# Optimization experiments

Hardware: AMD Instinct MI355X
Metric: run time of the kernel (lower is better)

The kernel has to match this reference:

```python
import jax, jax.numpy as jnp
import numpy as np
import math

DIM = 2048; H = 16; QR = 1536; KVR = 512; DN = 128; DR = 64; DV = 128
BS = 4; S = 1024
QK_HEAD = DN + DR  # 192


def _rms(x, w, eps=1e-6):
    v = jnp.mean(x * x, axis=-1, keepdims=True)
    return w * (x * jax.lax.rsqrt(v + eps))


def _rope_cos_sin(seq_len, dim):
    inv_freq = 1.0 / (10000.0 ** (jnp.arange(0, dim, 2, dtype=jnp.float32) / dim))
    t = jnp.arange(seq_len, dtype=jnp.float32)
    freqs = jnp.einsum('s,d->sd', t, inv_freq)
    freqs = jnp.concatenate([freqs, freqs], axis=-1)  # [S, dim]
    return jnp.cos(freqs), jnp.sin(freqs)


def _rotate_half(x):
    x1, x2 = jnp.split(x, 2, axis=-1)
    return jnp.concatenate([-x2, x1], axis=-1)


def setup_inputs() -> dict:
    key = jax.random.key(0)
    ks = jax.random.split(key, 12)
    sd = 0.02
    x = jax.random.normal(ks[0], (BS, S, DIM), dtype=jnp.float32)
    # causal additive mask [b, s, t]
    i = jnp.arange(S)
    causal = jnp.where(i[:, None] >= i[None, :], 0.0, -1e9).astype(jnp.float32)
    mask = jnp.broadcast_to(causal, (BS, S, S))
    return {
        'x': x,
        'mask': mask,
        'wq_a_w': jax.random.normal(ks[1], (QR, DIM)) * sd,
        'wq_a_b': jnp.zeros((QR,), jnp.float32),
        'q_norm_w': jnp.ones((QR,), jnp.float32),
        'wq_b_w': jax.random.normal(ks[2], (H * QK_HEAD, QR)) * sd,
        'wq_b_b': jnp.zeros((H * QK_HEAD,), jnp.float32),
        'wkv_a_w': jax.random.normal(ks[3], (KVR + DR, DIM)) * sd,
        'wkv_a_b': jnp.zeros((KVR + DR,), jnp.float32),
        'kv_norm_w': jnp.ones((KVR,), jnp.float32),
        'wkv_b_w': jax.random.normal(ks[4], (H * (DN + DV), KVR)) * sd,
        'wo_w': jax.random.normal(ks[5], (DIM, H * DV)) * sd,
        'wo_b': jnp.zeros((DIM,), jnp.float32),
    }


def reference(x, mask, wq_a_w, wq_a_b, q_norm_w, wq_b_w, wq_b_b,
              wkv_a_w, wkv_a_b, kv_norm_w, wkv_b_w, wo_w, wo_b):
    bs, seq_len, _ = x.shape
    # Q low-rank path
    q = x @ wq_a_w.T + wq_a_b                     # [b,s,QR]
    q = _rms(q, q_norm_w)
    q = q @ wq_b_w.T + wq_b_b                     # [b,s,H*192]
    q = q.reshape(bs, seq_len, H, QK_HEAD)
    q_nope, q_pe = q[..., :DN], q[..., DN:]       # [b,s,h,128], [b,s,h,64]
    # compressed KV path
    kv = x @ wkv_a_w.T + wkv_a_b                  # [b,s,KVR+64]
    c, k_pe = kv[..., :KVR], kv[..., KVR:]        # [b,s,512], [b,s,64]
    # RoPE on the rope sub-dims
    cos, sin = _rope_cos_sin(seq_len, DR)         # [s,64]
    cos4 = cos[None, :, None, :]
    sin4 = sin[None, :, None, :]
    q_pe = q_pe * cos4 + _rotate_half(q_pe) * sin4
    k_pe4 = k_pe[:, :, None, :]
    k_pe = (k_pe4 * cos4 + _rotate_half(k_pe4) * sin4)[:, :, 0, :]  # [b,s,64]
    # weight absorption: wkv_b viewed [H, DN+DV, KVR]
    wkv_b = wkv_b_w.reshape(H, DN + DV, KVR)
    q_abs = jnp.einsum('bshd,hdc->bshc', q_nope, wkv_b[:, :DN])      # [b,s,h,512]
    c_n = _rms(c, kv_norm_w)                                         # [b,t,512]
    scores = (jnp.einsum('bshc,btc->bsht', q_abs, c_n)
              + jnp.einsum('bshr,btr->bsht', q_pe, k_pe)) / math.sqrt(QK_HEAD)
    scores = scores + mask[:, :, None, :]
    scores = jax.nn.softmax(scores, axis=-1)
    o = jnp.einsum('bsht,btc->bshc', scores, c_n)                    # [b,s,h,512]
    o = jnp.einsum('bshc,hdc->bshd', o, wkv_b[:, -DV:])              # [b,s,h,128]
    o = o.reshape(bs, seq_len, H * DV)
    return o @ wo_w.T + wo_b
```

## Files before the change

### kernel.cpp

```cpp
#include <hip/hip_runtime.h>


typedef __attribute__((ext_vector_type(8))) short bf16x8;
typedef __attribute__((ext_vector_type(4))) float f32x4;
typedef __attribute__((ext_vector_type(4))) int i32x4;
typedef unsigned short ushort_t;
typedef unsigned int uint32;

typedef const __attribute__((address_space(1))) void* gas_ptr;
typedef __attribute__((address_space(3))) void* las_ptr;

#define DEV __device__ __forceinline__
#define WAITVM(N) asm volatile("s_waitcnt vmcnt(" #N ")" ::: "memory")

DEV float b2f(ushort_t u) { return __uint_as_float(((uint32)u) << 16); }
DEV ushort_t f2b(float f) {
  uint32 u = __float_as_uint(f);
  return (ushort_t)((u + 0x7fffu + ((u >> 16) & 1u)) >> 16);
}
DEV uint32 pkb(float lo, float hi) { return (uint32)f2b(lo) | ((uint32)f2b(hi) << 16); }

DEV void c4seg(const float4* __restrict__ in, ushort4* __restrict__ out, int i, int n4) {
  if (i < n4) {
    float4 v = in[i];
    ushort4 o; o.x = f2b(v.x); o.y = f2b(v.y); o.z = f2b(v.z); o.w = f2b(v.w);
    out[i] = o;
  }
}
DEV void vbseg(const float* __restrict__ in, ushort_t* __restrict__ out, int i4, int dofs) {
  int c4 = i4 & 127, d = (i4 >> 7) & 127, h = i4 >> 14;
  const float4 v = *(const float4*)(in + ((long)(h * 256 + dofs + d)) * 512 + c4 * 4);
  ushort4 o; o.x = f2b(v.x); o.y = f2b(v.y); o.z = f2b(v.z); o.w = f2b(v.w);
  ((ushort4*)out)[i4] = o;
}
__global__ __launch_bounds__(256) void castall_k(
    const float* __restrict__ x, const float* __restrict__ wq_a_w,
    const float* __restrict__ wkv_a_w, const float* __restrict__ wq_b_w,
    const float* __restrict__ wo_w, const float* __restrict__ wkv_b_w,
    ushort_t* __restrict__ xb, ushort_t* __restrict__ wcomb,
    ushort_t* __restrict__ wqb, ushort_t* __restrict__ wo,
    ushort_t* __restrict__ wkvbv, ushort_t* __restrict__ wkvbn) {
  int blk = blockIdx.x, tid = threadIdx.x;
  if (blk < 8192) {
    c4seg((const float4*)x, (ushort4*)xb, blk * 256 + tid, 2097152);
  } else if (blk < 11264) {
    c4seg((const float4*)wq_a_w, (ushort4*)wcomb, (blk - 8192) * 256 + tid, 786432);
  } else if (blk < 12416) {
    c4seg((const float4*)wkv_a_w, (ushort4*)(wcomb + 1536 * 2048),
          (blk - 11264) * 256 + tid, 294912);
  } else if (blk < 17024) {
    c4seg((const float4*)wq_b_w, (ushort4*)wqb, (blk - 12416) * 256 + tid, 1179648);
  } else if (blk < 21120) {
    c4seg((const float4*)wo_w, (ushort4*)wo, (blk - 17024) * 256 + tid, 1048576);
  } else if (blk < 22144) {
    vbseg(wkv_b_w, wkvbv, (blk - 21120) * 256 + tid, 128);
  } else {
    vbseg(wkv_b_w, wkvbn, (blk - 22144) * 256 + tid, 0);
  }
}

DEV float block_reduce_sum(float v, float* sbuf) {
#pragma unroll
  for (int d = 32; d >= 1; d >>= 1) v += __shfl_xor(v, d);
  if ((threadIdx.x & 63) == 0) sbuf[threadIdx.x >> 6] = v;
  __syncthreads();
  return sbuf[0] + sbuf[1] + sbuf[2] + sbuf[3];
}

__global__ __launch_bounds__(256) void rms_1536_k(const float* __restrict__ in,
                                                  ushort_t* __restrict__ out,
                                                  const float* __restrict__ w) {
  __shared__ float sbuf[4];
  long row = blockIdx.x;
  const float* p = in + row * 1536;
  float v[6]; float ss = 0.f;
#pragma unroll
  for (int i = 0; i < 6; ++i) { v[i] = p[threadIdx.x + i * 256]; ss += v[i] * v[i]; }
  ss = block_reduce_sum(ss, sbuf);
  float sc = rsqrtf(ss * (1.0f / 1536.0f) + 1e-6f);
#pragma unroll
  for (int i = 0; i < 6; ++i) {
    int c = threadIdx.x + i * 256;
    out[row * 1536 + c] = f2b(v[i] * sc * w[c]);
  }
}

__global__ __launch_bounds__(512) void kvfuse_k(const float* __restrict__ kvf,
                                                const float* __restrict__ w,
                                                ushort_t* __restrict__ kcat,
                                                ushort_t* __restrict__ vtp,
                                                ushort_t* __restrict__ kabs) {
  __shared__ ushort_t sh[8 * 512];
  int tid = threadIdx.x, wv = tid >> 6, lane = tid & 63;
  long row = (long)blockIdx.x * 8 + wv;
  const float* p = kvf + row * 576;
  float4 v0 = *(const float4*)(p + lane * 8);
  float4 v1 = *(const float4*)(p + lane * 8 + 4);
  float ss = v0.x * v0.x + v0.y * v0.y + v0.z * v0.z + v0.w * v0.w
           + v1.x * v1.x + v1.y * v1.y + v1.z * v1.z + v1.w * v1.w;
#pragma unroll
  for (int d = 1; d <= 32; d <<= 1) ss += __shfl_xor(ss, d);
  float sc = rsqrtf(ss * (1.0f / 512.0f) + 1e-6f);
  float4 w0 = *(const float4*)(w + lane * 8);
  float4 w1 = *(const float4*)(w + lane * 8 + 4);
  ushort_t tmp[8];
  tmp[0] = f2b(v0.x * sc * w0.x); tmp[1] = f2b(v0.y * sc * w0.y);
  tmp[2] = f2b(v0.z * sc * w0.z); tmp[3] = f2b(v0.w * sc * w0.w);
  tmp[4] = f2b(v1.x * sc * w1.x); tmp[5] = f2b(v1.y * sc * w1.y);
  tmp[6] = f2b(v1.z * sc * w1.z); tmp[7] = f2b(v1.w * sc * w1.w);
  *(uint4*)(kcat + row * 576 + lane * 8) = *(uint4*)tmp;
  *(uint4*)(sh + wv * 512 + lane * 8) = *(uint4*)tmp;
  if (lane < 32) {
    int t = (int)(row & 1023);
    float x1 = p[512 + lane], x2 = p[544 + lane];
    float ang = (float)t * powf(10000.0f, -(float)lane * (1.0f / 32.0f));
    float s, c; sincosf(ang, &s, &c);
    ushort_t r1 = f2b(x1 * c - x2 * s), r2 = f2b(x2 * c + x1 * s);
    kcat[row * 576 + 512 + lane] = r1;
    kcat[row * 576 + 544 + lane] = r2;
#pragma unroll
    for (int h = 0; h < 16; ++h) {
      long base = ((long)h * 4096 + row) * 192;
      kabs[base + 128 + lane] = r1;
      kabs[base + 160 + lane] = r2;
    }
  }
  __syncthreads();
  ushort_t t8[8];
#pragma unroll
  for (int j = 0; j < 8; ++j) t8[j] = sh[j * 512 + tid];
  int b = blockIdx.x >> 7, tb = blockIdx.x & 127;
  *(uint4*)(vtp + (((long)b * 128 + tb) * 512 + tid) * 8) = *(uint4*)t8;
}

template <bool OUT_BF16>
__global__ __launch_bounds__(256) void gemm_bt_k(
    const ushort_t* __restrict__ A, int lda, long sAz,
    const ushort_t* __restrict__ B, int ldb, long sBz,
    void* __restrict__ C, int ldc, long sCz,
    const float* __restrict__ bias, float scale,
    int M, int N, int K) {
  __shared__ ushort_t As[2 * 4096];
  __shared__ ushort_t Bs[2 * 4096];
  int tid = threadIdx.x;
  int wave = tid >> 6, lane = tid & 63;
  int row0 = blockIdx.x * 128, col0 = blockIdx.y * 128;
  int z = blockIdx.z;
  const ushort_t* Az = A + (long)z * sAz;
  const ushort_t* Bz = B + (long)z * sBz;
  int wr = wave >> 1, wc = wave & 1;
  int lr = lane & 15, kq = lane >> 4;

  f32x4 acc[4][4];
#pragma unroll
  for (int m = 0; m < 4; ++m)
#pragma unroll
    for (int n = 0; n < 4; ++n) acc[m][n] = (f32x4){0.f, 0.f, 0.f, 0.f};

  auto stage = [&](int buf, int k0) {
#pragma unroll
    for (int rnd = 0; rnd < 2; ++rnd) {
      int e = rnd * 2048 + wave * 512 + lane * 8;
      int tr = e >> 5, tc = e & 31;
      int ar = row0 + tr; if (ar >= M) ar = M - 1;
      int br = col0 + tr; if (br >= N) br = N - 1;
      __builtin_amdgcn_global_load_lds((gas_ptr)(Az + (long)ar * lda + (k0 + tc)),
          (las_ptr)(As + buf * 4096 + rnd * 2048 + wave * 512), 16, 0, 0);
      __builtin_amdgcn_global_load_lds((gas_ptr)(Bz + (long)br * ldb + (k0 + tc)),
          (las_ptr)(Bs + buf * 4096 + rnd * 2048 + wave * 512), 16, 0, 0);
    }
  };

  stage(0, 0);
  int nk = K >> 5;
  for (int kt = 0; kt < nk; ++kt) {
    int cur = kt & 1;
    if (kt + 1 < nk) { stage(cur ^ 1, (kt + 1) * 32); WAITVM(4); }
    else { WAITVM(0); }
    __builtin_amdgcn_s_barrier();
    __builtin_amdgcn_sched_barrier(0);
    const ushort_t* Ac = As + cur * 4096;
    const ushort_t* Bc = Bs + cur * 4096;
    bf16x8 a[4], bb[4];
#pragma unroll
    for (int m = 0; m < 4; ++m)
      a[m] = *(const bf16x8*)(Ac + (wr * 64 + m * 16 + lr) * 32 + kq * 8);
#pragma unroll
    for (int n = 0; n < 4; ++n)
      bb[n] = *(const bf16x8*)(Bc + (wc * 64 + n * 16 + lr) * 32 + kq * 8);
#pragma unroll
    for (int m = 0; m < 4; ++m)
#pragma unroll
      for (int n = 0; n < 4; ++n)
        acc[m][n] = __builtin_amdgcn_mfma_f32_16x16x32_bf16(bb[n], a[m], acc[m][n], 0, 0, 0);
    __builtin_amdgcn_s_barrier();
  }

#pragma unroll
  for (int m = 0; m < 4; ++m) {
    int gr = row0 + wr * 64 + m * 16 + lr;
    if (gr >= M) continue;
#pragma unroll
    for (int n = 0; n < 4; ++n) {
      int cb = col0 + wc * 64 + n * 16 + kq * 4;
      if (cb >= N) continue;
      f32x4 v = acc[m][n];
#pragma unroll
      for (int r = 0; r < 4; ++r) v[r] = v[r] * scale + (bias ? bias[cb + r] : 0.f);
      long ci = (long)z * sCz + (long)gr * ldc + cb;
      if constexpr (OUT_BF16) {
        ushort4 pk; pk.x = f2b(v[0]); pk.y = f2b(v[1]); pk.z = f2b(v[2]); pk.w = f2b(v[3]);
        *(ushort4*)((ushort_t*)C + ci) = pk;
      } else {
        *(f32x4*)((float*)C + ci) = v;
      }
    }
  }
}

template <int MODE>
__global__ __launch_bounds__(256) void gemm64_k(
    const ushort_t* __restrict__ A, int lda,
    const ushort_t* __restrict__ B, int ldb,
    void* __restrict__ C, int ldc,
    const float* __restrict__ bias,
    void* __restrict__ C2, const float* __restrict__ bias2,
    int M, int N, int K) {
  __shared__ ushort_t As[2 * 8192];
  __shared__ ushort_t Bs[2 * 8192];
  int tid = threadIdx.x;
  int wave = tid >> 6, lane = tid & 63;
  int bid = blockIdx.y * gridDim.x + blockIdx.x;
  int nwg = gridDim.x * gridDim.y;
  int swz = (bid & 7) * (nwg >> 3) + (bid >> 3);
  int bx = swz % gridDim.x, by = swz / gridDim.x;
  int row0 = bx * 128, col0 = by * 128;
  int wr = wave >> 1, wc = wave & 1;
  int lr = lane & 15, kq = lane >> 4;
  int rsw = lr & 7;

  f32x4 acc[4][4];
#pragma unroll
  for (int m = 0; m < 4; ++m)
#pragma unroll
    for (int n = 0; n < 4; ++n) acc[m][n] = (f32x4){0.f, 0.f, 0.f, 0.f};

  auto stage = [&](int buf, int k0) {
#pragma unroll
    for (int ii = 0; ii < 4; ++ii) {
      int e = ii * 256 + tid;
      int r = e >> 3, c = e & 7;
      int scol = ((c ^ (r & 7)) << 3);
      int ar = row0 + r; if (ar >= M) ar = M - 1;
      int br = col0 + r; if (br >= N) br = N - 1;
      __builtin_amdgcn_global_load_lds((gas_ptr)(A + (long)ar * lda + k0 + scol),
          (las_ptr)(As + buf * 8192 + e * 8), 16, 0, 0);
      __builtin_amdgcn_global_load_lds((gas_ptr)(B + (long)br * ldb + k0 + scol),
          (las_ptr)(Bs + buf * 8192 + e * 8), 16, 0, 0);
    }
  };

  stage(0, 0);
  int nk = K >> 6;
  for (int kt = 0; kt < nk; ++kt) {
    int cur = kt & 1;
    if (kt + 1 < nk) { stage(cur ^ 1, (kt + 1) * 64); WAITVM(8); }
    else { WAITVM(0); }
    __builtin_amdgcn_s_barrier();
    __builtin_amdgcn_sched_barrier(0);
    const ushort_t* Ac = As + cur * 8192;
    const ushort_t* Bc = Bs + cur * 8192;
#pragma unroll
    for (int ks = 0; ks < 2; ++ks) {
      bf16x8 a[4], bb[4];
#pragma unroll
      for (int m = 0; m < 4; ++m) {
        int row = wr * 64 + m * 16 + lr;
        a[m] = *(const bf16x8*)(Ac + row * 64 + ((((ks << 2) | kq) ^ rsw) << 3));
      }
#pragma unroll
      for (int n = 0; n < 4; ++n) {
        int row = wc * 64 + n * 16 + lr;
        bb[n] = *(const bf16x8*)(Bc + row * 64 + ((((ks << 2) | kq) ^ rsw) << 3));
      }
#pragma unroll
      for (int m = 0; m < 4; ++m)
#pragma unroll
        for (int n = 0; n < 4; ++n)
          acc[m][n] = __builtin_amdgcn_mfma_f32_16x16x32_bf16(bb[n], a[m], acc[m][n], 0, 0, 0);
    }
    __builtin_amdgcn_s_barrier();
  }

  if constexpr (MODE == 0) {
#pragma unroll
    for (int m = 0; m < 4; ++m) {
      int gr = row0 + wr * 64 + m * 16 + lr;
      if (gr >= M) continue;
#pragma unroll
      for (int n = 0; n < 4; ++n) {
        int cb = col0 + wc * 64 + n * 16 + kq * 4;
        if (cb >= N) continue;
        f32x4 v = acc[m][n];
#pragma unroll
        for (int r = 0; r < 4; ++r) v[r] += bias[cb + r];
        *(f32x4*)((float*)C + (long)gr * ldc + cb) = v;
      }
    }
  } else if constexpr (MODE == 1) {
#pragma unroll
    for (int m = 0; m < 4; ++m) {
      int gr = row0 + wr * 64 + m * 16 + lr;
      if (gr >= M) continue;
#pragma unroll
      for (int n = 0; n < 4; ++n) {
        int cb = col0 + wc * 64 + n * 16 + kq * 4;
        if (cb >= N) continue;
        f32x4 v = acc[m][n];
        if (cb < 1536) {
#pragma unroll
          for (int r = 0; r < 4; ++r) v[r] += bias[cb + r];
          *(f32x4*)((float*)C + (long)gr * 1536 + cb) = v;
        } else {
          int c2 = cb - 1536;
#pragma unroll
          for (int r = 0; r < 4; ++r) v[r] += bias2[c2 + r];
          *(f32x4*)((float*)C2 + (long)gr * 576 + c2) = v;
        }
      }
    }
  } else {
    const float RS = 0.07216878364870322f;
#pragma unroll
    for (int n = 0; n < 4; ++n) {
      int cb = col0 + wc * 64 + n * 16 + kq * 4;
      int h = cb / 192, d0 = cb - h * 192;
      ushort_t* qh = (ushort_t*)C + (long)h * 4096 * 192;
      if (d0 < 128) {
        f32x4 bv; 
#pragma unroll
        for (int r = 0; r < 4; ++r) bv[r] = bias[cb + r];
#pragma unroll
        for (int m = 0; m < 4; ++m) {
          int gr = row0 + wr * 64 + m * 16 + lr;
          f32x4 v = acc[m][n];
          ushort4 pk;
          pk.x = f2b((v[0] + bv[0]) * RS); pk.y = f2b((v[1] + bv[1]) * RS);
          pk.z = f2b((v[2] + bv[2]) * RS); pk.w = f2b((v[3] + bv[3]) * RS);
          *(ushort4*)(qh + (long)gr * 192 + d0) = pk;
        }
      } else if (d0 < 160) {
        int nn = (n < 2) ? n : 0;
        f32x4 bv1, bv2, invf;
#pragma unroll
        for (int r = 0; r < 4; ++r) {
          bv1[r] = bias[cb + r]; bv2[r] = bias[cb + 32 + r];
          invf[r] = powf(10000.0f, -(float)(d0 - 128 + r) * (1.0f / 32.0f));
        }
#pragma unroll
        for (int m = 0; m < 4; ++m) {
          int gr = row0 + wr * 64 + m * 16 + lr;
          int t = gr & 1023;
          f32x4 v1 = acc[m][nn], v2 = acc[m][nn + 2];
          ushort4 p1, p2;
#pragma unroll
          for (int r = 0; r < 4; ++r) {
            float s, c; sincosf((float)t * invf[r], &s, &c);
            float x1 = v1[r] + bv1[r], x2 = v2[r] + bv2[r];
            ((ushort_t*)&p1)[r] = f2b((x1 * c - x2 * s) * RS);
            ((ushort_t*)&p2)[r] = f2b((x2 * c + x1 * s) * RS);
          }
          *(ushort4*)(qh + (long)gr * 192 + d0) = p1;
          *(ushort4*)(qh + (long)gr * 192 + d0 + 32) = p2;
        }
      }
    }
  }
}

__global__ __launch_bounds__(512, 1) void flash5_k(const ushort_t* __restrict__ qcat2,
                                                   const ushort_t* __restrict__ kabs,
                                                   const ushort_t* __restrict__ vtp,
                                                   ushort_t* __restrict__ O) {
  __shared__ __align__(16) ushort_t SMEM[2 * 6400 + 2 * 16384];

  int tid = threadIdx.x;
  int wave = tid >> 6, lane = tid & 63;
  int lr = lane & 15, kq = lane >> 4;
  int bi = blockIdx.x;
  int jz = bi >> 6;
  int qb = (jz < 4) ? jz : 11 - jz;
  int bh = bi & 63;
  int h = bh >> 2, b = bh & 3;
  int s0 = qb * 128;
  int nt = (qb + 1) * 4;

  const ushort_t* kt = kabs + ((long)h * 4096 + b * 1024) * 192;
  const ushort_t* vt = vtp + (long)b * 524288;
  const ushort_t* qp = qcat2 + ((long)(h * 4096 + b * 1024 + s0 + wave * 16 + lr)) * 192 + kq * 8;

  auto stageK = [&](int buf, int t0) {
    const ushort_t* sb = kt + (long)t0 * 192;
    ushort_t* kb = SMEM + buf * 6400;
#pragma unroll
    for (int ii = 0; ii < 2; ++ii) {
      int c = ii * 512 + tid;
      if (ii == 1 && tid >= 288) break;
      int t = (int)((unsigned)c / 25u);
      int r = c - t * 25;
      int rr = (r == 24) ? 0 : r;
      const ushort_t* src = sb + t * 192 + rr * 8;
      __builtin_amdgcn_global_load_lds((gas_ptr)src, (las_ptr)(kb + c * 8), 16, 0, 0);
    }
  };
  auto stageV = [&](int buf, int t0) {
    const ushort_t* sb = vt + (long)(t0 >> 3) * 4096;
    ushort_t* vb = SMEM + 12800 + buf * 16384;
#pragma unroll
    for (int ii = 0; ii < 4; ++ii) {
      int c0 = (ii * 8 + wave) * 64;
      const ushort_t* src = sb + (long)(c0 + lane) * 8;
      __builtin_amdgcn_global_load_lds((gas_ptr)src, (las_ptr)(vb + c0 * 8), 16, 0, 0);
    }
  };

  stageK(0, 0); stageV(0, 0);
  bf16x8 qreg[6];
#pragma unroll
  for (int st = 0; st < 6; ++st) qreg[st] = *(const bf16x8*)(qp + st * 32);

  f32x4 o[32];
#pragma unroll
  for (int v = 0; v < 32; ++v) o[v] = (f32x4){0.f, 0.f, 0.f, 0.f};
  float m_run = -1e30f, l_run = 0.f;

  int row_g = s0 + wave * 16 + lr;
  int idx_lo = (((kq & 1) << 5) + lr) << 2;
  int idx_hi = idx_lo + 64;
  bool losel = (kq < 2);

  __syncthreads();

  for (int it = 0; it < nt; ++it) {
    int cur = it & 1;
    if (it + 1 < nt) { stageK(cur ^ 1, (it + 1) * 32); stageV(cur ^ 1, (it + 1) * 32); }
    const ushort_t* Kc = SMEM + cur * 6400;
    f32x4 sv0 = (f32x4){0.f, 0.f, 0.f, 0.f}, sv1 = sv0;
    __builtin_amdgcn_s_setprio(1);
#pragma unroll
    for (int st = 0; st < 6; ++st) {
      int off = st * 32 + kq * 8;
      bf16x8 k0 = *(const bf16x8*)(Kc + lr * 200 + off);
      bf16x8 k1 = *(const bf16x8*)(Kc + (16 + lr) * 200 + off);
      sv0 = __builtin_amdgcn_mfma_f32_16x16x32_bf16(k0, qreg[st], sv0, 0, 0, 0);
      sv1 = __builtin_amdgcn_mfma_f32_16x16x32_bf16(k1, qreg[st], sv1, 0, 0, 0);
    }
    __builtin_amdgcn_s_setprio(0);
    int t0 = it * 32;
    if (t0 >= s0) {
#pragma unroll
      for (int rr = 0; rr < 4; ++rr) {
        if (t0 + kq * 4 + rr > row_g) sv0[rr] = -1e30f;
        if (t0 + 16 + kq * 4 + rr > row_g) sv1[rr] = -1e30f;
      }
    }
    float mx = fmaxf(fmaxf(fmaxf(sv0[0], sv0[1]), fmaxf(sv0[2], sv0[3])),
                     fmaxf(fmaxf(sv1[0], sv1[1]), fmaxf(sv1[2], sv1[3])));
    mx = fmaxf(mx, __shfl_xor(mx, 16));
    mx = fmaxf(mx, __shfl_xor(mx, 32));
    float mn = (mx > m_run + 8.0f) ? mx : m_run;
    float alpha = __expf(m_run - mn);
    float p0 = __expf(sv0[0] - mn), p1 = __expf(sv0[1] - mn);
    float p2 = __expf(sv0[2] - mn), p3 = __expf(sv0[3] - mn);
    float p4 = __expf(sv1[0] - mn), p5 = __expf(sv1[1] - mn);
    float p6 = __expf(sv1[2] - mn), p7 = __expf(sv1[3] - mn);
    float psum = ((p0 + p1) + (p2 + p3)) + ((p4 + p5) + (p6 + p7));
    psum += __shfl_xor(psum, 16);
    psum += __shfl_xor(psum, 32);
    l_run = l_run * alpha + psum;
    m_run = mn;
    int u0 = (int)pkb(p0, p1), u1 = (int)pkb(p2, p3);
    int u2 = (int)pkb(p4, p5), u3 = (int)pkb(p6, p7);
    int b00 = __builtin_amdgcn_ds_bpermute(idx_lo, u0);
    int b10 = __builtin_amdgcn_ds_bpermute(idx_lo, u1);
    int b20 = __builtin_amdgcn_ds_bpermute(idx_lo, u2);
    int b30 = __builtin_amdgcn_ds_bpermute(idx_lo, u3);
    int b01 = __builtin_amdgcn_ds_bpermute(idx_hi, u0);
    int b11 = __builtin_amdgcn_ds_bpermute(idx_hi, u1);
    int b21 = __builtin_amdgcn_ds_bpermute(idx_hi, u2);
    int b31 = __builtin_amdgcn_ds_bpermute(idx_hi, u3);
    i32x4 w;
    w.x = losel ? b00 : b20; w.y = losel ? b10 : b30;
    w.z = losel ? b01 : b21; w.w = losel ? b11 : b31;
    bf16x8 pa = __builtin_bit_cast(bf16x8, w);
    float a0 = __shfl(alpha, kq * 4 + 0), a1 = __shfl(alpha, kq * 4 + 1);
    float a2 = __shfl(alpha, kq * 4 + 2), a3 = __shfl(alpha, kq * 4 + 3);
    if (__any((a0 != 1.f) | (a1 != 1.f) | (a2 != 1.f) | (a3 != 1.f))) {
      f32x4 av; av[0] = a0; av[1] = a1; av[2] = a2; av[3] = a3;
#pragma unroll
      for (int v = 0; v < 32; ++v) o[v] *= av;
    }
    const ushort_t* Vc = SMEM + 12800 + cur * 16384 + (kq * 512 + lr) * 8;
    __builtin_amdgcn_s_setprio(1);
#pragma unroll
    for (int v = 0; v < 32; ++v) {
      bf16x8 bv = *(const bf16x8*)(Vc + v * 128);
      o[v] = __builtin_amdgcn_mfma_f32_16x16x32_bf16(pa, bv, o[v], 0, 0, 0);
    }
    __builtin_amdgcn_s_setprio(0);
    __syncthreads();
  }
  float l0 = __shfl(l_run, kq * 4 + 0), l1 = __shfl(l_run, kq * 4 + 1);
  float l2 = __shfl(l_run, kq * 4 + 2), l3 = __shfl(l_run, kq * 4 + 3);
  f32x4 inv; inv[0] = 1.f / l0; inv[1] = 1.f / l1; inv[2] = 1.f / l2; inv[3] = 1.f / l3;
  ushort_t* ob = O + ((long)(h * 4096 + b * 1024 + s0 + wave * 16 + kq * 4)) * 512 + lr;
#pragma unroll
  for (int rr = 0; rr < 4; ++rr) {
    ushort_t* orow = ob + (long)rr * 512;
#pragma unroll
    for (int v = 0; v < 32; ++v) orow[v * 16] = f2b(o[v][rr] * inv[rr]);
  }
}

extern "C" void kernel_launch(void* const* d_in, const int* in_sizes, int n_in,
                              void* d_out, int out_size, void* d_ws, size_t ws_size,
                              hipStream_t stream) {
  (void)in_sizes; (void)n_in;
  const float* x         = (const float*)d_in[0];
  const float* wq_a_w    = (const float*)d_in[2];
  const float* wq_a_b    = (const float*)d_in[3];
  const float* q_norm_w  = (const float*)d_in[4];
  const float* wq_b_w    = (const float*)d_in[5];
  const float* wq_b_b    = (const float*)d_in[6];
  const float* wkv_a_w   = (const float*)d_in[7];
  const float* wkv_a_b   = (const float*)d_in[8];
  const float* kv_norm_w = (const float*)d_in[9];
  const float* wkv_b_w   = (const float*)d_in[10];
  const float* wo_w      = (const float*)d_in[11];
  const float* wo_b      = (const float*)d_in[12];

  char* ws = (char*)d_ws;
  constexpr size_t OFF_XB     = 0;
  constexpr size_t OFF_WCOMB  = 16777216;
  constexpr size_t OFF_WQB    = 25427968;
  constexpr size_t OFF_QA     = 34865152;
  constexpr size_t OFF_QAN    = 60030976;
  constexpr size_t OFF_QCAT2  = 72613888;
  constexpr size_t OFF_WKVBN  = 97779712;
  constexpr size_t OFF_WKVBV  = 99876864;
  constexpr size_t OFF_WO     = 101974016;
  constexpr size_t OFF_KVF    = 110362624;
  constexpr size_t OFF_KCAT   = 119799808;
  constexpr size_t OFF_VTP    = 124518400;
  constexpr size_t OFF_KABS   = 128712704;
  constexpr size_t OFF_O      = 153878528;
  constexpr size_t OFF_O2     = 220987392;
  constexpr size_t WS_NEED    = 237764608;
  if (ws_size < WS_NEED) {
    (void)hipMemsetAsync(d_out, 0, (size_t)out_size * sizeof(float), stream);
    return;
  }

  ushort_t* xb     = (ushort_t*)(ws + OFF_XB);
  ushort_t* wcomb  = (ushort_t*)(ws + OFF_WCOMB);
  ushort_t* wqb    = (ushort_t*)(ws + OFF_WQB);
  float*    qa     = (float*)(ws + OFF_QA);
  ushort_t* qan    = (ushort_t*)(ws + OFF_QAN);
  ushort_t* qcat2  = (ushort_t*)(ws + OFF_QCAT2);
  ushort_t* wkvbn  = (ushort_t*)(ws + OFF_WKVBN);
  ushort_t* wkvbv  = (ushort_t*)(ws + OFF_WKVBV);
  ushort_t* wo     = (ushort_t*)(ws + OFF_WO);
  float*    kvf    = (float*)(ws + OFF_KVF);
  ushort_t* kcat   = (ushort_t*)(ws + OFF_KCAT);
  ushort_t* vtp    = (ushort_t*)(ws + OFF_VTP);
  ushort_t* kabs   = (ushort_t*)(ws + OFF_KABS);
  ushort_t* Obuf   = (ushort_t*)(ws + OFF_O);
  ushort_t* o2     = (ushort_t*)(ws + OFF_O2);

  castall_k<<<23168, 256, 0, stream>>>(x, wq_a_w, wkv_a_w, wq_b_w, wo_w, wkv_b_w,
                                       xb, wcomb, wqb, wo, wkvbv, wkvbn);
  gemm64_k<1><<<dim3(32, 17), 256, 0, stream>>>(xb, 2048, wcomb, 2048,
      qa, 1536, wq_a_b, kvf, wkv_a_b, 4096, 2112, 2048);
  rms_1536_k<<<4096, 256, 0, stream>>>(qa, qan, q_norm_w);
  gemm64_k<2><<<dim3(32, 24), 256, 0, stream>>>(qan, 1536, wqb, 1536,
      qcat2, 0, wq_b_b, nullptr, nullptr, 4096, 3072, 1536);
  kvfuse_k<<<512, 512, 0, stream>>>(kvf, kv_norm_w, kcat, vtp, kabs);
  gemm_bt_k<true><<<dim3(32, 1, 16), 256, 0, stream>>>(kcat, 576, 0,
      wkvbn, 512, (long)128 * 512, kabs, 192, (long)4096 * 192,
      nullptr, 1.f, 4096, 128, 512);
  flash5_k<<<512, 512, 0, stream>>>(qcat2, kabs, vtp, Obuf);
  gemm_bt_k<true><<<dim3(32, 1, 16), 256, 0, stream>>>(Obuf, 512, (long)4096 * 512,
      wkvbv, 512, (long)128 * 512, o2, 2048, 128, nullptr, 1.f, 4096, 128, 512);
  gemm64_k<0><<<dim3(32, 16), 256, 0, stream>>>(o2, 2048, wo, 2048,
      (float*)d_out, 2048, wo_b, nullptr, nullptr, 4096, 2048, 2048);
}
```

Baseline: 378.8 us.

## Fuse RMS-norm kernels and single-buffer K tile in flash attention

Merges the q RMS-norm and the kv norm/rope/transpose kernels into one launch using a block-index split. In the attention kernel, the K shared-memory tile goes from double-buffered to single-buffered. The next K/V prefetch is now issued after the score MFMAs finish, behind an explicit lgkm wait and barrier, and the end-of-iteration sync becomes a vmcnt wait plus barrier. The launch bound is raised to allow 4 blocks per CU. This cuts LDS use to raise occupancy and removes one launch, at the cost of less overlap between K loading and the QK compute.

```diff
diff --git a/kernel.cpp b/kernel.cpp
--- a/kernel.cpp
+++ b/kernel.cpp
@@ -12,6 +12,7 @@
 
 #define DEV __device__ __forceinline__
 #define WAITVM(N) asm volatile("s_waitcnt vmcnt(" #N ")" ::: "memory")
+#define WAITLGKM0 asm volatile("s_waitcnt lgkmcnt(0)" ::: "memory")
 
 DEV float b2f(ushort_t u) { return __uint_as_float(((uint32)u) << 16); }
 DEV ushort_t f2b(float f) {
@@ -59,78 +60,76 @@
   }
 }
 
-DEV float block_reduce_sum(float v, float* sbuf) {
-#pragma unroll
-  for (int d = 32; d >= 1; d >>= 1) v += __shfl_xor(v, d);
-  if ((threadIdx.x & 63) == 0) sbuf[threadIdx.x >> 6] = v;
-  __syncthreads();
-  return sbuf[0] + sbuf[1] + sbuf[2] + sbuf[3];
-}
-
-__global__ __launch_bounds__(256) void rms_1536_k(const float* __restrict__ in,
-                                                  ushort_t* __restrict__ out,
-                                                  const float* __restrict__ w) {
-  __shared__ float sbuf[4];
-  long row = blockIdx.x;
-  const float* p = in + row * 1536;
-  float v[6]; float ss = 0.f;
-#pragma unroll
-  for (int i = 0; i < 6; ++i) { v[i] = p[threadIdx.x + i * 256]; ss += v[i] * v[i]; }
-  ss = block_reduce_sum(ss, sbuf);
-  float sc = rsqrtf(ss * (1.0f / 1536.0f) + 1e-6f);
-#pragma unroll
-  for (int i = 0; i < 6; ++i) {
-    int c = threadIdx.x + i * 256;
-    out[row * 1536 + c] = f2b(v[i] * sc * w[c]);
-  }
-}
-
-__global__ __launch_bounds__(512) void kvfuse_k(const float* __restrict__ kvf,
-                                                const float* __restrict__ w,
-                                                ushort_t* __restrict__ kcat,
-                                                ushort_t* __restrict__ vtp,
-                                                ushort_t* __restrict__ kabs) {
+__global__ __launch_bounds__(512) void rmskv_k(const float* __restrict__ qa_in,
+                                               ushort_t* __restrict__ qan,
+                                               const float* __restrict__ q_norm_w,
+                                               const float* __restrict__ kvf,
+                                               const float* __restrict__ kv_norm_w,
+                                               ushort_t* __restrict__ kcat,
+                                               ushort_t* __restrict__ vtp,
+                                               ushort_t* __restrict__ kabs) {
+  __shared__ float sbuf[8];
   __shared__ ushort_t sh[8 * 512];
-  int tid = threadIdx.x, wv = tid >> 6, lane = tid & 63;
-  long row = (long)blockIdx.x * 8 + wv;
-  const float* p = kvf + row * 576;
-  float4 v0 = *(const float4*)(p + lane * 8);
-  float4 v1 = *(const float4*)(p + lane * 8 + 4);
-  float ss = v0.x * v0.x + v0.y * v0.y + v0.z * v0.z + v0.w * v0.w
-           + v1.x * v1.x + v1.y * v1.y + v1.z * v1.z + v1.w * v1.w;
-#pragma unroll
-  for (int d = 1; d <= 32; d <<= 1) ss += __shfl_xor(ss, d);
-  float sc = rsqrtf(ss * (1.0f / 512.0f) + 1e-6f);
-  float4 w0 = *(const float4*)(w + lane * 8);
-  float4 w1 = *(const float4*)(w + lane * 8 + 4);
-  ushort_t tmp[8];
-  tmp[0] = f2b(v0.x * sc * w0.x); tmp[1] = f2b(v0.y * sc * w0.y);
-  tmp[2] = f2b(v0.z * sc * w0.z); tmp[3] = f2b(v0.w * sc * w0.w);
-  tmp[4] = f2b(v1.x * sc * w1.x); tmp[5] = f2b(v1.y * sc * w1.y);
-  tmp[6] = f2b(v1.z * sc * w1.z); tmp[7] = f2b(v1.w * sc * w1.w);
-  *(uint4*)(kcat + row * 576 + lane * 8) = *(uint4*)tmp;
-  *(uint4*)(sh + wv * 512 + lane * 8) = *(uint4*)tmp;
-  if (lane < 32) {
-    int t = (int)(row & 1023);
-    float x1 = p[512 + lane], x2 = p[544 + lane];
-    float ang = (float)t * powf(10000.0f, -(float)lane * (1.0f / 32.0f));
-    float s, c; sincosf(ang, &s, &c);
-    ushort_t r1 = f2b(x1 * c - x2 * s), r2 = f2b(x2 * c + x1 * s);
-    kcat[row * 576 + 512 + lane] = r1;
-    kcat[row * 576 + 544 + lane] = r2;
-#pragma unroll
-    for (int h = 0; h < 16; ++h) {
-      long base = ((long)h * 4096 + row) * 192;
-      kabs[base + 128 + lane] = r1;
-      kabs[base + 160 + lane] = r2;
-    }
-  }
-  __syncthreads();
-  ushort_t t8[8];
-#pragma unroll
-  for (int j = 0; j < 8; ++j) t8[j] = sh[j * 512 + tid];
-  int b = blockIdx.x >> 7, tb = blockIdx.x & 127;
-  *(uint4*)(vtp + (((long)b * 128 + tb) * 512 + tid) * 8) = *(uint4*)t8;
+  int blk = blockIdx.x, tid = threadIdx.x;
+  int wv = tid >> 6, lane = tid & 63;
+  if (blk < 4096) {
+    long row = blk;
+    const float* p = qa_in + row * 1536;
+    float v0 = p[tid], v1 = p[tid + 512], v2 = p[tid + 1024];
+    float ss = v0 * v0 + v1 * v1 + v2 * v2;
+#pragma unroll
+    for (int d = 1; d <= 32; d <<= 1) ss += __shfl_xor(ss, d);
+    if (lane == 0) sbuf[wv] = ss;
+    __syncthreads();
+    float tot = 0.f;
+#pragma unroll
+    for (int i = 0; i < 8; ++i) tot += sbuf[i];
+    float sc = rsqrtf(tot * (1.0f / 1536.0f) + 1e-6f);
+    qan[row * 1536 + tid] = f2b(v0 * sc * q_norm_w[tid]);
+    qan[row * 1536 + tid + 512] = f2b(v1 * sc * q_norm_w[tid + 512]);
+    qan[row * 1536 + tid + 1024] = f2b(v2 * sc * q_norm_w[tid + 1024]);
+  } else {
+    int kb = blk - 4096;
+    long row = (long)kb * 8 + wv;
+    const float* p = kvf + row * 576;
+    float4 v0 = *(const float4*)(p + lane * 8);
+    float4 v1 = *(const float4*)(p + lane * 8 + 4);
+    float ss = v0.x * v0.x + v0.y * v0.y + v0.z * v0.z + v0.w * v0.w
+             + v1.x * v1.x + v1.y * v1.y + v1.z * v1.z + v1.w * v1.w;
+#pragma unroll
+    for (int d = 1; d <= 32; d <<= 1) ss += __shfl_xor(ss, d);
+    float sc = rsqrtf(ss * (1.0f / 512.0f) + 1e-6f);
+    float4 w0 = *(const float4*)(kv_norm_w + lane * 8);
+    float4 w1 = *(const float4*)(kv_norm_w + lane * 8 + 4);
+    ushort_t tmp[8];
+    tmp[0] = f2b(v0.x * sc * w0.x); tmp[1] = f2b(v0.y * sc * w0.y);
+    tmp[2] = f2b(v0.z * sc * w0.z); tmp[3] = f2b(v0.w * sc * w0.w);
+    tmp[4] = f2b(v1.x * sc * w1.x); tmp[5] = f2b(v1.y * sc * w1.y);
+    tmp[6] = f2b(v1.z * sc * w1.z); tmp[7] = f2b(v1.w * sc * w1.w);
+    *(uint4*)(kcat + row * 576 + lane * 8) = *(uint4*)tmp;
+    *(uint4*)(sh + wv * 512 + lane * 8) = *(uint4*)tmp;
+    if (lane < 32) {
+      int t = (int)(row & 1023);
+      float x1 = p[512 + lane], x2 = p[544 + lane];
+      float ang = (float)t * powf(10000.0f, -(float)lane * (1.0f / 32.0f));
+      float s, c; sincosf(ang, &s, &c);
+      ushort_t r1 = f2b(x1 * c - x2 * s), r2 = f2b(x2 * c + x1 * s);
+      kcat[row * 576 + 512 + lane] = r1;
+      kcat[row * 576 + 544 + lane] = r2;
+#pragma unroll
+      for (int h = 0; h < 16; ++h) {
+        long base = ((long)h * 4096 + row) * 192;
+        kabs[base + 128 + lane] = r1;
+        kabs[base + 160 + lane] = r2;
+      }
+    }
+    __syncthreads();
+    ushort_t t8[8];
+#pragma unroll
+    for (int j = 0; j < 8; ++j) t8[j] = sh[j * 512 + tid];
+    int b = kb >> 7, tb = kb & 127;
+    *(uint4*)(vtp + (((long)b * 128 + tb) * 512 + tid) * 8) = *(uint4*)t8;
+  }
 }
 
 template <bool OUT_BF16>
@@ -337,7 +336,7 @@
       int h = cb / 192, d0 = cb - h * 192;
       ushort_t* qh = (ushort_t*)C + (long)h * 4096 * 192;
       if (d0 < 128) {
-        f32x4 bv; 
+        f32x4 bv;
 #pragma unroll
         for (int r = 0; r < 4; ++r) bv[r] = bias[cb + r];
 #pragma unroll
@@ -378,11 +377,11 @@
   }
 }
 
-__global__ __launch_bounds__(512, 1) void flash5_k(const ushort_t* __restrict__ qcat2,
+__global__ __launch_bounds__(512, 4) void flash7_k(const ushort_t* __restrict__ qcat2,
                                                    const ushort_t* __restrict__ kabs,
                                                    const ushort_t* __restrict__ vtp,
                                                    ushort_t* __restrict__ O) {
-  __shared__ __align__(16) ushort_t SMEM[2 * 6400 + 2 * 16384];
+  __shared__ __align__(16) ushort_t SMEM[6400 + 2 * 16384];
 
   int tid = threadIdx.x;
   int wave = tid >> 6, lane = tid & 63;
@@ -399,9 +398,8 @@
   const ushort_t* vt = vtp + (long)b * 524288;
   const ushort_t* qp = qcat2 + ((long)(h * 4096 + b * 1024 + s0 + wave * 16 + lr)) * 192 + kq * 8;
 
-  auto stageK = [&](int buf, int t0) {
+  auto stageK = [&](int t0) {
     const ushort_t* sb = kt + (long)t0 * 192;
-    ushort_t* kb = SMEM + buf * 6400;
 #pragma unroll
     for (int ii = 0; ii < 2; ++ii) {
       int c = ii * 512 + tid;
@@ -410,12 +408,12 @@
       int r = c - t * 25;
       int rr = (r == 24) ? 0 : r;
       const ushort_t* src = sb + t * 192 + rr * 8;
-      __builtin_amdgcn_global_load_lds((gas_ptr)src, (las_ptr)(kb + c * 8), 16, 0, 0);
+      __builtin_amdgcn_global_load_lds((gas_ptr)src, (las_ptr)(SMEM + c * 8), 16, 0, 0);
     }
   };
   auto stageV = [&](int buf, int t0) {
     const ushort_t* sb = vt + (long)(t0 >> 3) * 4096;
-    ushort_t* vb = SMEM + 12800 + buf * 16384;
+    ushort_t* vb = SMEM + 6400 + buf * 16384;
 #pragma unroll
     for (int ii = 0; ii < 4; ++ii) {
       int c0 = (ii * 8 + wave) * 64;
@@ -424,7 +422,7 @@
     }
   };
 
-  stageK(0, 0); stageV(0, 0);
+  stageK(0); stageV(0, 0);
   bf16x8 qreg[6];
 #pragma unroll
   for (int st = 0; st < 6; ++st) qreg[st] = *(const bf16x8*)(qp + st * 32);
@@ -443,19 +441,21 @@
 
   for (int it = 0; it < nt; ++it) {
     int cur = it & 1;
-    if (it + 1 < nt) { stageK(cur ^ 1, (it + 1) * 32); stageV(cur ^ 1, (it + 1) * 32); }
-    const ushort_t* Kc = SMEM + cur * 6400;
     f32x4 sv0 = (f32x4){0.f, 0.f, 0.f, 0.f}, sv1 = sv0;
     __builtin_amdgcn_s_setprio(1);
 #pragma unroll
     for (int st = 0; st < 6; ++st) {
       int off = st * 32 + kq * 8;
-      bf16x8 k0 = *(const bf16x8*)(Kc + lr * 200 + off);
-      bf16x8 k1 = *(const bf16x8*)(Kc + (16 + lr) * 200 + off);
+      bf16x8 k0 = *(const bf16x8*)(SMEM + lr * 200 + off);
+      bf16x8 k1 = *(const bf16x8*)(SMEM + (16 + lr) * 200 + off);
       sv0 = __builtin_amdgcn_mfma_f32_16x16x32_bf16(k0, qreg[st], sv0, 0, 0, 0);
       sv1 = __builtin_amdgcn_mfma_f32_16x16x32_bf16(k1, qreg[st], sv1, 0, 0, 0);
     }
     __builtin_amdgcn_s_setprio(0);
+    WAITLGKM0;
+    __builtin_amdgcn_sched_barrier(0);
+    __builtin_amdgcn_s_barrier();
+    if (it + 1 < nt) { stageK((it + 1) * 32); stageV(cur ^ 1, (it + 1) * 32); }
     int t0 = it * 32;
     if (t0 >= s0) {
 #pragma unroll
@@ -500,7 +500,7 @@
 #pragma unroll
       for (int v = 0; v < 32; ++v) o[v] *= av;
     }
-    const ushort_t* Vc = SMEM + 12800 + cur * 16384 + (kq * 512 + lr) * 8;
+    const ushort_t* Vc = SMEM + 6400 + cur * 16384 + (kq * 512 + lr) * 8;
     __builtin_amdgcn_s_setprio(1);
 #pragma unroll
     for (int v = 0; v < 32; ++v) {
@@ -508,7 +508,8 @@
       o[v] = __builtin_amdgcn_mfma_f32_16x16x32_bf16(pa, bv, o[v], 0, 0, 0);
     }
     __builtin_amdgcn_s_setprio(0);
-    __syncthreads();
+    WAITVM(0);
+    __builtin_amdgcn_s_barrier();
   }
   float l0 = __shfl(l_run, kq * 4 + 0), l1 = __shfl(l_run, kq * 4 + 1);
   float l2 = __shfl(l_run, kq * 4 + 2), l3 = __shfl(l_run, kq * 4 + 3);
@@ -581,14 +582,13 @@
                                        xb, wcomb, wqb, wo, wkvbv, wkvbn);
   gemm64_k<1><<<dim3(32, 17), 256, 0, stream>>>(xb, 2048, wcomb, 2048,
       qa, 1536, wq_a_b, kvf, wkv_a_b, 4096, 2112, 2048);
-  rms_1536_k<<<4096, 256, 0, stream>>>(qa, qan, q_norm_w);
+  rmskv_k<<<4608, 512, 0, stream>>>(qa, qan, q_norm_w, kvf, kv_norm_w, kcat, vtp, kabs);
   gemm64_k<2><<<dim3(32, 24), 256, 0, stream>>>(qan, 1536, wqb, 1536,
       qcat2, 0, wq_b_b, nullptr, nullptr, 4096, 3072, 1536);
-  kvfuse_k<<<512, 512, 0, stream>>>(kvf, kv_norm_w, kcat, vtp, kabs);
   gemm_bt_k<true><<<dim3(32, 1, 16), 256, 0, stream>>>(kcat, 576, 0,
       wkvbn, 512, (long)128 * 512, kabs, 192, (long)4096 * 192,
       nullptr, 1.f, 4096, 128, 512);
-  flash5_k<<<512, 512, 0, stream>>>(qcat2, kabs, vtp, Obuf);
+  flash7_k<<<512, 512, 0, stream>>>(qcat2, kabs, vtp, Obuf);
   gemm_bt_k<true><<<dim3(32, 1, 16), 256, 0, stream>>>(Obuf, 512, (long)4096 * 512,
       wkvbv, 512, (long)128 * 512, o2, 2048, 128, nullptr, 1.f, 4096, 128, 512);
   gemm64_k<0><<<dim3(32, 16), 256, 0, stream>>>(o2, 2048, wo, 2048,
```

Result: slower. 1.152 ms (+204.0%).
